# Kernel optimization log

Measured on AMD Instinct MI355X. Metric: run time of the kernel, lower is better.

Reference implementation:

```python
import jax, jax.numpy as jnp
import numpy as np

T, B, D, K = 256, 128, 1024, 21
PAD = 0


def setup_inputs() -> dict:
    key = jax.random.key(0)
    k1, k2, k3, k4, k5, k6, k7 = jax.random.split(key, 7)
    lstm_features = jax.random.normal(k1, (T, B, D), dtype=jnp.float32)
    # gold tags: non-pad (1..K-1) for a random prefix, PAD afterwards; mask[0] all on
    tags = jax.random.randint(k2, (T, B), 1, K)
    lengths = jax.random.randint(k3, (B,), T // 2, T + 1)
    tags = jnp.where(jnp.arange(T)[:, None] < lengths[None, :], tags, PAD)
    W = jax.random.normal(k4, (D, K), dtype=jnp.float32) * 0.02
    b = jnp.zeros((K,), dtype=jnp.float32)
    # torchcrf initializes transitions uniform(-0.1, 0.1)
    start_transitions = jax.random.uniform(k5, (K,), minval=-0.1, maxval=0.1)
    end_transitions = jax.random.uniform(k6, (K,), minval=-0.1, maxval=0.1)
    transitions = jax.random.uniform(k7, (K, K), minval=-0.1, maxval=0.1)
    return {
        'lstm_features': lstm_features,
        'tags': tags,
        'W': W,
        'b': b,
        'start_transitions': start_transitions,
        'end_transitions': end_transitions,
        'transitions': transitions,
    }


def _crf_nll(emissions, tags, mask, start, end, trans):
    # emissions: (T,B,K), tags/mask: (T,B). Returns -sum_b log p(tags|emissions)
    maskf = mask.astype(emissions.dtype)
    # --- numerator: score of gold path (fully vectorized over t) ---
    em_score = jnp.take_along_axis(emissions, tags[:, :, None], axis=2)[:, :, 0]  # (T,B)
    tr_score = trans[tags[:-1], tags[1:]]                                          # (T-1,B)
    num = start[tags[0]] + em_score[0]
    num = num + jnp.sum((tr_score + em_score[1:]) * maskf[1:], axis=0)
    seq_ends = jnp.sum(mask.astype(jnp.int32), axis=0) - 1                         # (B,)
    last_tags = jnp.take_along_axis(tags, seq_ends[None, :], axis=0)[0]
    num = num + end[last_tags]
    # --- denominator: forward algorithm (log partition) via scan ---
    def step(score, xs):  # score: (B,K)
        emit_t, mask_t = xs
        nxt = jax.nn.logsumexp(score[:, :, None] + trans[None, :, :] + emit_t[:, None, :], axis=1)
        return jnp.where(mask_t[:, None], nxt, score), None
    score0 = start[None, :] + emissions[0]
    scoreT, _ = jax.lax.scan(step, score0, (emissions[1:], mask[1:]))
    den = jax.nn.logsumexp(scoreT + end[None, :], axis=1)                          # (B,)
    return -jnp.sum(num - den)


def _viterbi(emissions, mask, start, end, trans):
    # returns best tag sequence (T,B) int32, padded positions set to PAD
    n_tags = emissions.shape[-1]
    ident = jnp.arange(n_tags, dtype=jnp.int32)[None, :]
    def step(score, xs):  # score: (B,K)
        emit_t, mask_t = xs
        cand = score[:, :, None] + trans[None, :, :]          # (B, prev K, next K)
        best_prev = jnp.argmax(cand, axis=1).astype(jnp.int32)  # (B,K)
        nxt = jnp.max(cand, axis=1) + emit_t
        ptr = jnp.where(mask_t[:, None], best_prev, ident)    # identity ptr on padding
        new_score = jnp.where(mask_t[:, None], nxt, score)
        return new_score, ptr
    score0 = start[None, :] + emissions[0]
    scoreT, history = jax.lax.scan(step, score0, (emissions[1:], mask[1:]))  # history: (T-1,B,K)
    last_tag = jnp.argmax(scoreT + end[None, :], axis=1).astype(jnp.int32)   # (B,)
    def back(tag, hist_t):
        prev = jnp.take_along_axis(hist_t, tag[:, None], axis=1)[:, 0]
        return prev, tag
    first_tag, rest = jax.lax.scan(back, last_tag, history, reverse=True)    # rest = tags[1:]
    best = jnp.concatenate([first_tag[None, :], rest], axis=0)               # (T,B)
    return jnp.where(mask, best, PAD)


def reference(lstm_features, tags, W, b, start_transitions, end_transitions, transitions):
    # Linear projection; dropout is identity at inference
    fc_out = jnp.einsum('tbd,dk->tbk', lstm_features, W) + b
    mask = tags != PAD
    crf_out = _viterbi(fc_out, mask, start_transitions, end_transitions, transitions)
    crf_loss = _crf_nll(fc_out, tags, mask, start_transitions, end_transitions, transitions)
    return crf_out, crf_loss
```

## Files before the change

### kernel.cpp

```cpp
#include <hip/hip_runtime.h>
#include <math.h>

#define T_ 256
#define B_ 128
#define D_ 1024
#define K_ 21
#define NB3 43

typedef short v8s __attribute__((ext_vector_type(8)));
typedef float v4f __attribute__((ext_vector_type(4)));

__device__ __forceinline__ short bf16rne(float f) {
  unsigned u = __float_as_uint(f);
  u += 0x7FFFu + ((u >> 16) & 1u);
  return (short)(u >> 16);
}
__device__ __forceinline__ float rdl(float v, int l) {
  return __int_as_float(__builtin_amdgcn_readlane(__float_as_int(v), l));
}
__device__ __forceinline__ int imax3(int a, int b, int c) {
  const int t = a > b ? a : b;
  return t > c ? t : c;
}

typedef const __attribute__((address_space(1))) void* gas1_t;
typedef __attribute__((address_space(3))) void* las3_t;
__device__ __forceinline__ void gload_lds(const float* g, float* l) {
  __builtin_amdgcn_global_load_lds((gas1_t)g, (las3_t)l, 4, 0, 0);
}

__global__ __launch_bounds__(256) void fc_kernel(
    const float* __restrict__ A, const float* __restrict__ W,
    const float* __restrict__ bias, float* __restrict__ fc,
    float* __restrict__ out_loss) {
  __shared__ float red[3][64][22];
  if (blockIdx.x == 0 && threadIdx.x == 0) *out_loss = 0.f;
  const int lane = threadIdx.x & 63;
  const int wv = threadIdx.x >> 6;
  const int m15 = lane & 15, g4 = lane >> 4;
  const int rowbase = blockIdx.x * 64;
  const int kc = wv * 256;
  const int n1 = 16 + m15;

  v8s bf[8][2];
#pragma unroll
  for (int s = 0; s < 8; ++s) {
    const float* Wp = W + (size_t)(kc + 32 * s + 8 * g4) * K_;
#pragma unroll
    for (int j = 0; j < 8; ++j) bf[s][0][j] = bf16rne(Wp[j * K_ + m15]);
    if (n1 < K_) {
#pragma unroll
      for (int j = 0; j < 8; ++j) bf[s][1][j] = bf16rne(Wp[j * K_ + n1]);
    } else {
#pragma unroll
      for (int j = 0; j < 8; ++j) bf[s][1][j] = 0;
    }
  }

  v4f acc[4][2];
#pragma unroll
  for (int m = 0; m < 4; ++m) {
    acc[m][0] = (v4f)(0.f);
    acc[m][1] = (v4f)(0.f);
  }

#pragma unroll
  for (int s = 0; s < 8; ++s) {
    v8s av[4];
#pragma unroll
    for (int m = 0; m < 4; ++m) {
      const float* Ap =
          A + (size_t)(rowbase + 16 * m + m15) * D_ + kc + 32 * s + 8 * g4;
      const float4 x = *(const float4*)Ap;
      const float4 y = *(const float4*)(Ap + 4);
      av[m][0] = bf16rne(x.x); av[m][1] = bf16rne(x.y);
      av[m][2] = bf16rne(x.z); av[m][3] = bf16rne(x.w);
      av[m][4] = bf16rne(y.x); av[m][5] = bf16rne(y.y);
      av[m][6] = bf16rne(y.z); av[m][7] = bf16rne(y.w);
    }
#pragma unroll
    for (int m = 0; m < 4; ++m) {
      acc[m][0] = __builtin_amdgcn_mfma_f32_16x16x32_bf16(av[m], bf[s][0],
                                                          acc[m][0], 0, 0, 0);
      acc[m][1] = __builtin_amdgcn_mfma_f32_16x16x32_bf16(av[m], bf[s][1],
                                                          acc[m][1], 0, 0, 0);
    }
  }

  if (wv > 0) {
#pragma unroll
    for (int m = 0; m < 4; ++m)
#pragma unroll
      for (int ri = 0; ri < 4; ++ri) {
        const int rl = 16 * m + 4 * g4 + ri;
        red[wv - 1][rl][m15] = acc[m][0][ri];
        if (n1 < K_) red[wv - 1][rl][n1] = acc[m][1][ri];
      }
  }
  __syncthreads();
  if (wv == 0) {
    const float b0 = bias[m15];
    const float b1 = (n1 < K_) ? bias[n1] : 0.f;
#pragma unroll
    for (int m = 0; m < 4; ++m)
#pragma unroll
      for (int ri = 0; ri < 4; ++ri) {
        const int rl = 16 * m + 4 * g4 + ri;
        float* o = fc + (size_t)(rowbase + rl) * K_;
        o[m15] = acc[m][0][ri] + red[0][rl][m15] + red[1][rl][m15] +
                 red[2][rl][m15] + b0;
        if (n1 < K_)
          o[n1] = acc[m][1][ri] + red[0][rl][n1] + red[1][rl][n1] +
                  red[2][rl][n1] + b1;
      }
  }
}

__global__ __launch_bounds__(64) void scan_kernel(
    const float* __restrict__ fc, const int* __restrict__ tags,
    const float* __restrict__ startT, const float* __restrict__ endT,
    const float* __restrict__ trans, float* __restrict__ out_tags,
    float* __restrict__ out_loss) {
  __shared__ v4f statev[18];
  __shared__ float fcs[2][32][64];
  __shared__ unsigned short bp[256 * 66];
  __shared__ unsigned char h2[127 * 66];
  __shared__ unsigned char h4[63 * 66];
  __shared__ unsigned char cur[3 * 256];

  const int lane = threadIdx.x;
  const int blk = blockIdx.x;

  if (blk < 2 * NB3) {
    const bool fwd = blk < NB3;
    const int bblk = fwd ? blk : blk - NB3;
    int g = lane / 21;
    if (g > 2) g = 2;
    int jloc = lane - g * 21;
    if (jloc > 20) jloc = 20;
    const int gj = g * 21 + jloc;
    const int b0 = bblk * 3;

    int len0 = 0, len1 = 0, len2 = 0;
#pragma unroll
    for (int q = 0; q < 4; ++q) {
      const int t = q * 64 + lane;
      int bb0 = b0, bb1 = b0 + 1, bb2 = b0 + 2;
      if (bb1 >= B_) bb1 = B_ - 1;
      if (bb2 >= B_) bb2 = B_ - 1;
      len0 += __popcll(__ballot(tags[t * B_ + bb0] != 0));
      len1 += __popcll(__ballot(tags[t * B_ + bb1] != 0));
      len2 += __popcll(__ballot(tags[t * B_ + bb2] != 0));
    }
    const int mylen = (g == 0) ? len0 : (g == 1) ? len1 : len2;

    float* sb = (float*)statev + g * 24;
    const v4f* sv = (const v4f*)sb;

#define STAGE(c)                                                             \
    {                                                                        \
      const float* src_ = fc + ((size_t)((c) * 32) * B_ + b0) * K_ + lane;   \
      float* dst_ = &fcs[(c) & 1][0][0];                                     \
      _Pragma("unroll")                                                      \
      for (int q_ = 0; q_ < 32; ++q_)                                        \
        gload_lds(src_ + (size_t)q_ * (B_ * K_), dst_ + q_ * 64);            \
    }
#define WAIT_VM0()                                                           \
    {                                                                        \
      asm volatile("s_waitcnt vmcnt(0)" ::: "memory");                       \
      __builtin_amdgcn_sched_barrier(0);                                     \
    }

    STAGE(0)
    WAIT_VM0()
    const float em0 = fcs[0][0][gj];
    STAGE(1)

    if (fwd) {
      float ec[21];
#pragma unroll
      for (int i = 0; i < K_; ++i) ec[i] = __expf(trans[i * K_ + jloc]);
      float p = __expf(startT[jloc] + em0);
      sb[jloc] = p;
      float L = 0.f;

      for (int c = 0; c < 8; ++c) {
        const float* fb = &fcs[c & 1][0][0];
        const int t1 = c * 32 + 32;
        for (int t = c ? c * 32 : 1; t < t1; ++t) {
          const float emt = fb[(t & 31) * 64 + gj];
          const v4f A0 = sv[0], A1 = sv[1], A2 = sv[2], A3 = sv[3],
                    A4 = sv[4];
          const float A5 = sb[20];

          float d0 = A0[0] * ec[0], d1 = A0[1] * ec[1], d2 = A0[2] * ec[2];
          d0 = fmaf(A0[3], ec[3], d0); d1 = fmaf(A1[0], ec[4], d1);
          d2 = fmaf(A1[1], ec[5], d2);
          d0 = fmaf(A1[2], ec[6], d0); d1 = fmaf(A1[3], ec[7], d1);
          d2 = fmaf(A2[0], ec[8], d2);
          d0 = fmaf(A2[1], ec[9], d0); d1 = fmaf(A2[2], ec[10], d1);
          d2 = fmaf(A2[3], ec[11], d2);
          d0 = fmaf(A3[0], ec[12], d0); d1 = fmaf(A3[1], ec[13], d1);
          d2 = fmaf(A3[2], ec[14], d2);
          d0 = fmaf(A3[3], ec[15], d0); d1 = fmaf(A4[0], ec[16], d1);
          d2 = fmaf(A4[1], ec[17], d2);
          d0 = fmaf(A4[2], ec[18], d0); d1 = fmaf(A4[3], ec[19], d1);
          d2 = fmaf(A5, ec[20], d2);

          const float pn = ((d0 + d1) + d2) * __expf(emt);
          p = (t < mylen) ? pn : p;
          if ((t & 7) == 0) {
            const float f = A0[0];
            p *= __builtin_amdgcn_rcpf(f);
            L += __logf(f);
          }
          sb[jloc] = p;
        }
        if (c < 7) {
          WAIT_VM0()
          if (c + 2 < 8) STAGE(c + 2)
        }
      }

      const float w = p * __expf(endT[jloc]);
      float res = 0.f;
#pragma unroll
      for (int gg = 0; gg < 3; ++gg) {
        if (b0 + gg < B_) {
          float tot = 0.f;
#pragma unroll
          for (int i = 0; i < K_; ++i) tot += rdl(w, gg * K_ + i);
          res += rdl(L, gg * K_) + __logf(tot);
        }
      }
      if (lane == 0) atomicAdd(out_loss, res);
    } else {
      float tr[21];
#pragma unroll
      for (int i = 0; i < K_; ++i) tr[i] = trans[i * K_ + jloc] + 2048.0f;
      float sc = startT[jloc] + em0;
      sb[jloc] = sc;

      for (int c = 0; c < 8; ++c) {
        const float* fb = &fcs[c & 1][0][0];
        const int t1 = c * 32 + 32;
        for (int t = c ? c * 32 : 1; t < t1; ++t) {
          const float emt = fb[(t & 31) * 64 + gj];
          const v4f A0 = sv[0], A1 = sv[1], A2 = sv[2], A3 = sv[3],
                    A4 = sv[4];
          const float A5 = sb[20];

#define KEY(i, V) ((__float_as_int((V) + tr[i]) & 0xFFFFFFE0) | (20 - (i)))
          const int q0 = imax3(KEY(0, A0[0]), KEY(1, A0[1]), KEY(2, A0[2]));
          const int q1 = imax3(KEY(3, A0[3]), KEY(4, A1[0]), KEY(5, A1[1]));
          const int q2 = imax3(KEY(6, A1[2]), KEY(7, A1[3]), KEY(8, A2[0]));
          const int q3 = imax3(KEY(9, A2[1]), KEY(10, A2[2]), KEY(11, A2[3]));
          const int q4 = imax3(KEY(12, A3[0]), KEY(13, A3[1]), KEY(14, A3[2]));
          const int q5 = imax3(KEY(15, A3[3]), KEY(16, A4[0]), KEY(17, A4[1]));
          const int q6 = imax3(KEY(18, A4[2]), KEY(19, A4[3]), KEY(20, A5));
          const int km = imax3(imax3(q0, q1, q2), imax3(q3, q4, q5), q6);
#undef KEY
          const float nxt = __int_as_float(km & 0xFFFFFFE0) - 2048.0f + emt;
          const bool m = t < mylen;
          sc = m ? nxt : sc;
          sb[jloc] = sc;
          const int pw = m ? (20 - (km & 31)) : jloc;
          bp[t * 66 + g * 22 + jloc] = (unsigned short)pw;
        }
        if (c < 7) {
          WAIT_VM0()
          if (c + 2 < 8) STAGE(c + 2)
        }
      }
      __syncthreads();

      const float finb = sc + endT[jloc] + 2048.0f;
      const int myk = (__float_as_int(finb) & 0xFFFFFFE0) | (20 - jloc);
      int last0 = 0, last1 = 0, last2 = 0;
#pragma unroll
      for (int gg = 0; gg < 3; ++gg) {
        int km = 0;
#pragma unroll
        for (int i = 0; i < K_; ++i) {
          const int ki = __builtin_amdgcn_readlane(myk, gg * K_ + i);
          km = km > ki ? km : ki;
        }
        const int lt = 20 - (km & 31);
        if (gg == 0) last0 = lt;
        else if (gg == 1) last1 = lt;
        else last2 = lt;
      }

      for (int i = lane; i < 127 * 63; i += 64) {
        const int v = i / 63;
        const int rem = i - v * 63;
        const int gg = rem / 21, j = rem - (rem / 21) * 21;
        h2[v * 66 + gg * 22 + j] = (unsigned char)
            bp[(2 * v + 1) * 66 + gg * 22 + bp[(2 * v + 2) * 66 + gg * 22 + j]];
      }
      __syncthreads();
      for (int i = lane; i < 63 * 63; i += 64) {
        const int w = i / 63;
        const int rem = i - w * 63;
        const int gg = rem / 21, j = rem - (rem / 21) * 21;
        h4[w * 66 + gg * 22 + j] =
            h2[(2 * w) * 66 + gg * 22 + h2[(2 * w + 1) * 66 + gg * 22 + j]];
      }
      __syncthreads();

      if (lane < 3 && b0 + lane < B_) {
        int c = (lane == 0) ? last0 : (lane == 1) ? last1 : last2;
        cur[lane * 256 + 255] = (unsigned char)c;
        c = bp[255 * 66 + lane * 22 + c];
        cur[lane * 256 + 254] = (unsigned char)c;
        c = h2[126 * 66 + lane * 22 + c];
        cur[lane * 256 + 252] = (unsigned char)c;
        for (int w = 62; w >= 0; --w) {
          c = h4[w * 66 + lane * 22 + c];
          cur[lane * 256 + 4 * w] = (unsigned char)c;
        }
      }
      __syncthreads();
      for (int i = lane; i < 63 * 3; i += 64) {
        const int gg = i / 63, ii = i - (i / 63) * 63;
        const int t = 2 + 4 * ii;
        cur[gg * 256 + t] =
            h2[(t >> 1) * 66 + gg * 22 + cur[gg * 256 + t + 2]];
      }
      __syncthreads();
      for (int i = lane; i < 127 * 3; i += 64) {
        const int gg = i / 127, ii = i - (i / 127) * 127;
        const int t = 1 + 2 * ii;
        cur[gg * 256 + t] = (unsigned char)
            bp[(t + 1) * 66 + gg * 22 + cur[gg * 256 + t + 1]];
      }
      __syncthreads();
      for (int i = lane; i < 3 * 256; i += 64) {
        const int gg = i >> 8, t = i & 255;
        const int bb = b0 + gg;
        const int lg = (gg == 0) ? len0 : (gg == 1) ? len1 : len2;
        if (bb < B_)
          out_tags[t * B_ + bb] = (t < lg) ? (float)cur[gg * 256 + t] : 0.f;
      }
    }
#undef STAGE
#undef WAIT_VM0
  } else {
    const int b = blk - 2 * NB3;
    float contrib = 0.f;
#pragma unroll
    for (int q = 0; q < 4; ++q) {
      const int t = lane * 4 + q;
      const int tg = tags[t * B_ + b];
      const size_t ro = ((size_t)t * B_ + b) * K_;
      if (t == 0) {
        contrib += startT[tg] + fc[ro + tg];
      } else if (tg != 0) {
        const int pg = tags[(t - 1) * B_ + b];
        contrib += trans[pg * K_ + tg] + fc[ro + tg];
      }
      const bool isLast =
          (tg != 0) && (t == T_ - 1 || tags[(t + 1) * B_ + b] == 0);
      if (isLast) contrib += endT[tg];
    }
#pragma unroll
    for (int off = 32; off > 0; off >>= 1)
      contrib += __shfl_down(contrib, off, 64);
    if (lane == 0) atomicAdd(out_loss, -contrib);
  }
}

extern "C" void kernel_launch(void* const* d_in, const int* in_sizes, int n_in,
                              void* d_out, int out_size, void* d_ws,
                              size_t ws_size, hipStream_t stream) {
  const float* A = (const float*)d_in[0];
  const int* tags = (const int*)d_in[1];
  const float* W = (const float*)d_in[2];
  const float* bias = (const float*)d_in[3];
  const float* startT = (const float*)d_in[4];
  const float* endT = (const float*)d_in[5];
  const float* trans = (const float*)d_in[6];

  float* out_tags = (float*)d_out;
  float* out_loss = (float*)d_out + (size_t)T_ * B_;
  float* fc = (float*)d_ws;

  fc_kernel<<<512, 256, 0, stream>>>(A, W, bias, fc, out_loss);
  scan_kernel<<<2 * NB3 + B_, 64, 0, stream>>>(fc, tags, startT, endT, trans,
                                               out_tags, out_loss);
}
```

Measured before the change: 280.8 us.

## Fuse projection GEMM with CRF scans in one wave-specialized producer-consumer kernel

Replaces the separate projection kernel and scan kernel with a single kernel of 43 blocks. In each block, two waves compute the bf16 MFMA projection chunk by chunk into double-buffered LDS. Two other waves run the forward and Viterbi recurrences at the same time, synchronized through LDS flags. This removes the global round trip of the emission matrix and the second launch, and overlaps the memory-bound projection with the latency-bound serial scan. The cost is that the 128 MB input is now streamed by only 86 waves across 43 CUs. The loss reset also relies on a global magic-value flag that stays set from earlier calls, which may race on repeated launches.

New measurement: 486.0 us. 1.73x slower.

```diff
diff --git a/kernel.cpp b/kernel.cpp
--- a/kernel.cpp
+++ b/kernel.cpp
@@ -5,7 +5,8 @@
 #define B_ 128
 #define D_ 1024
 #define K_ 21
-#define NB3 43
+#define NBLK 43
+#define MAGIC64 0xA3C59B17E4D2F861ull
 
 typedef short v8s __attribute__((ext_vector_type(8)));
 typedef float v4f __attribute__((ext_vector_type(4)));
@@ -22,351 +23,358 @@
   const int t = a > b ? a : b;
   return t > c ? t : c;
 }
-
-typedef const __attribute__((address_space(1))) void* gas1_t;
-typedef __attribute__((address_space(3))) void* las3_t;
-__device__ __forceinline__ void gload_lds(const float* g, float* l) {
-  __builtin_amdgcn_global_load_lds((gas1_t)g, (las3_t)l, 4, 0, 0);
-}
-
-__global__ __launch_bounds__(256) void fc_kernel(
+__device__ __forceinline__ int cvt2(float lo, float hi) {
+  int r;
+  asm("v_cvt_pk_bf16_f32 %0, %1, %2" : "=v"(r) : "v"(lo), "v"(hi));
+  return r;
+}
+__device__ __forceinline__ void lds_wait(int* f) {
+  while (__hip_atomic_load(f, __ATOMIC_RELAXED, __HIP_MEMORY_SCOPE_WORKGROUP) == 0)
+    __builtin_amdgcn_s_sleep(1);
+}
+__device__ __forceinline__ void lds_set(int* f) {
+  __hip_atomic_store(f, 1, __ATOMIC_RELAXED, __HIP_MEMORY_SCOPE_WORKGROUP);
+}
+
+__global__ __launch_bounds__(256) void crf_kernel(
     const float* __restrict__ A, const float* __restrict__ W,
-    const float* __restrict__ bias, float* __restrict__ fc,
-    float* __restrict__ out_loss) {
-  __shared__ float red[3][64][22];
-  if (blockIdx.x == 0 && threadIdx.x == 0) *out_loss = 0.f;
-  const int lane = threadIdx.x & 63;
-  const int wv = threadIdx.x >> 6;
-  const int m15 = lane & 15, g4 = lane >> 4;
-  const int rowbase = blockIdx.x * 64;
-  const int kc = wv * 256;
-  const int n1 = 16 + m15;
-
-  v8s bf[8][2];
-#pragma unroll
-  for (int s = 0; s < 8; ++s) {
-    const float* Wp = W + (size_t)(kc + 32 * s + 8 * g4) * K_;
-#pragma unroll
-    for (int j = 0; j < 8; ++j) bf[s][0][j] = bf16rne(Wp[j * K_ + m15]);
-    if (n1 < K_) {
-#pragma unroll
-      for (int j = 0; j < 8; ++j) bf[s][1][j] = bf16rne(Wp[j * K_ + n1]);
-    } else {
-#pragma unroll
-      for (int j = 0; j < 8; ++j) bf[s][1][j] = 0;
-    }
-  }
-
-  v4f acc[4][2];
-#pragma unroll
-  for (int m = 0; m < 4; ++m) {
-    acc[m][0] = (v4f)(0.f);
-    acc[m][1] = (v4f)(0.f);
-  }
-
-#pragma unroll
-  for (int s = 0; s < 8; ++s) {
-    v8s av[4];
-#pragma unroll
-    for (int m = 0; m < 4; ++m) {
-      const float* Ap =
-          A + (size_t)(rowbase + 16 * m + m15) * D_ + kc + 32 * s + 8 * g4;
-      const float4 x = *(const float4*)Ap;
-      const float4 y = *(const float4*)(Ap + 4);
-      av[m][0] = bf16rne(x.x); av[m][1] = bf16rne(x.y);
-      av[m][2] = bf16rne(x.z); av[m][3] = bf16rne(x.w);
-      av[m][4] = bf16rne(y.x); av[m][5] = bf16rne(y.y);
-      av[m][6] = bf16rne(y.z); av[m][7] = bf16rne(y.w);
-    }
-#pragma unroll
-    for (int m = 0; m < 4; ++m) {
-      acc[m][0] = __builtin_amdgcn_mfma_f32_16x16x32_bf16(av[m], bf[s][0],
-                                                          acc[m][0], 0, 0, 0);
-      acc[m][1] = __builtin_amdgcn_mfma_f32_16x16x32_bf16(av[m], bf[s][1],
-                                                          acc[m][1], 0, 0, 0);
-    }
-  }
-
-  if (wv > 0) {
-#pragma unroll
-    for (int m = 0; m < 4; ++m)
-#pragma unroll
-      for (int ri = 0; ri < 4; ++ri) {
-        const int rl = 16 * m + 4 * g4 + ri;
-        red[wv - 1][rl][m15] = acc[m][0][ri];
-        if (n1 < K_) red[wv - 1][rl][n1] = acc[m][1][ri];
-      }
-  }
-  __syncthreads();
-  if (wv == 0) {
-    const float b0 = bias[m15];
-    const float b1 = (n1 < K_) ? bias[n1] : 0.f;
-#pragma unroll
-    for (int m = 0; m < 4; ++m)
-#pragma unroll
-      for (int ri = 0; ri < 4; ++ri) {
-        const int rl = 16 * m + 4 * g4 + ri;
-        float* o = fc + (size_t)(rowbase + rl) * K_;
-        o[m15] = acc[m][0][ri] + red[0][rl][m15] + red[1][rl][m15] +
-                 red[2][rl][m15] + b0;
-        if (n1 < K_)
-          o[n1] = acc[m][1][ri] + red[0][rl][n1] + red[1][rl][n1] +
-                  red[2][rl][n1] + b1;
-      }
-  }
-}
-
-__global__ __launch_bounds__(64) void scan_kernel(
-    const float* __restrict__ fc, const int* __restrict__ tags,
+    const float* __restrict__ bias, const int* __restrict__ tags,
     const float* __restrict__ startT, const float* __restrict__ endT,
     const float* __restrict__ trans, float* __restrict__ out_tags,
-    float* __restrict__ out_loss) {
-  __shared__ v4f statev[18];
+    float* __restrict__ out_loss, unsigned long long* __restrict__ readyg) {
   __shared__ float fcs[2][32][64];
+  __shared__ unsigned short Wt[21 * 1032];
   __shared__ unsigned short bp[256 * 66];
   __shared__ unsigned char h2[127 * 66];
   __shared__ unsigned char h4[63 * 66];
   __shared__ unsigned char cur[3 * 256];
-
-  const int lane = threadIdx.x;
+  __shared__ float stateF[3 * 24], stateV[3 * 24];
+  __shared__ int flg[5][8];
+
+  const int tix = threadIdx.x;
+  const int lane = tix & 63;
+  const int wv = tix >> 6;
   const int blk = blockIdx.x;
-
-  if (blk < 2 * NB3) {
-    const bool fwd = blk < NB3;
-    const int bblk = fwd ? blk : blk - NB3;
-    int g = lane / 21;
-    if (g > 2) g = 2;
-    int jloc = lane - g * 21;
-    if (jloc > 20) jloc = 20;
-    const int gj = g * 21 + jloc;
-    const int b0 = bblk * 3;
-
-    int len0 = 0, len1 = 0, len2 = 0;
-#pragma unroll
-    for (int q = 0; q < 4; ++q) {
-      const int t = q * 64 + lane;
-      int bb0 = b0, bb1 = b0 + 1, bb2 = b0 + 2;
-      if (bb1 >= B_) bb1 = B_ - 1;
-      if (bb2 >= B_) bb2 = B_ - 1;
-      len0 += __popcll(__ballot(tags[t * B_ + bb0] != 0));
-      len1 += __popcll(__ballot(tags[t * B_ + bb1] != 0));
-      len2 += __popcll(__ballot(tags[t * B_ + bb2] != 0));
-    }
-    const int mylen = (g == 0) ? len0 : (g == 1) ? len1 : len2;
-
-    float* sb = (float*)statev + g * 24;
+  const int b0 = blk * 3;
+
+  if (tix < 40) ((int*)flg)[tix] = 0;
+  if (blk == 0 && tix == 0) {
+    atomicExch(out_loss, 0.f);
+    __builtin_amdgcn_fence(__ATOMIC_RELEASE, "agent");
+    __hip_atomic_store(readyg, MAGIC64, __ATOMIC_RELAXED,
+                       __HIP_MEMORY_SCOPE_AGENT);
+  }
+  for (int i = tix; i < K_ * D_; i += 256) {
+    const int k = i / K_, c = i - (i / K_) * K_;
+    Wt[c * 1032 + k] = (unsigned short)bf16rne(W[i]);
+  }
+
+  int len0 = 0, len1 = 0, len2 = 0;
+#pragma unroll
+  for (int q = 0; q < 4; ++q) {
+    const int t = q * 64 + lane;
+    int bb0 = b0, bb1 = b0 + 1, bb2 = b0 + 2;
+    if (bb1 >= B_) bb1 = B_ - 1;
+    if (bb2 >= B_) bb2 = B_ - 1;
+    len0 += __popcll(__ballot(tags[t * B_ + bb0] != 0));
+    len1 += __popcll(__ballot(tags[t * B_ + bb1] != 0));
+    len2 += __popcll(__ballot(tags[t * B_ + bb2] != 0));
+  }
+  __syncthreads();
+
+  int g = lane / 21;
+  if (g > 2) g = 2;
+  int jloc = lane - g * 21;
+  if (jloc > 20) jloc = 20;
+  const int gj = g * 21 + jloc;
+  const int mylen = (g == 0) ? len0 : (g == 1) ? len1 : len2;
+  int last0 = 0, last1 = 0, last2 = 0;
+
+  if (wv == 0) {
+    float* sb = stateF + g * 24;
     const v4f* sv = (const v4f*)sb;
-
-#define STAGE(c)                                                             \
-    {                                                                        \
-      const float* src_ = fc + ((size_t)((c) * 32) * B_ + b0) * K_ + lane;   \
-      float* dst_ = &fcs[(c) & 1][0][0];                                     \
-      _Pragma("unroll")                                                      \
-      for (int q_ = 0; q_ < 32; ++q_)                                        \
-        gload_lds(src_ + (size_t)q_ * (B_ * K_), dst_ + q_ * 64);            \
-    }
-#define WAIT_VM0()                                                           \
-    {                                                                        \
-      asm volatile("s_waitcnt vmcnt(0)" ::: "memory");                       \
-      __builtin_amdgcn_sched_barrier(0);                                     \
-    }
-
-    STAGE(0)
-    WAIT_VM0()
-    const float em0 = fcs[0][0][gj];
-    STAGE(1)
-
-    if (fwd) {
-      float ec[21];
-#pragma unroll
-      for (int i = 0; i < K_; ++i) ec[i] = __expf(trans[i * K_ + jloc]);
-      float p = __expf(startT[jloc] + em0);
-      sb[jloc] = p;
-      float L = 0.f;
-
-      for (int c = 0; c < 8; ++c) {
-        const float* fb = &fcs[c & 1][0][0];
-        const int t1 = c * 32 + 32;
-        for (int t = c ? c * 32 : 1; t < t1; ++t) {
-          const float emt = fb[(t & 31) * 64 + gj];
-          const v4f A0 = sv[0], A1 = sv[1], A2 = sv[2], A3 = sv[3],
-                    A4 = sv[4];
-          const float A5 = sb[20];
-
-          float d0 = A0[0] * ec[0], d1 = A0[1] * ec[1], d2 = A0[2] * ec[2];
-          d0 = fmaf(A0[3], ec[3], d0); d1 = fmaf(A1[0], ec[4], d1);
-          d2 = fmaf(A1[1], ec[5], d2);
-          d0 = fmaf(A1[2], ec[6], d0); d1 = fmaf(A1[3], ec[7], d1);
-          d2 = fmaf(A2[0], ec[8], d2);
-          d0 = fmaf(A2[1], ec[9], d0); d1 = fmaf(A2[2], ec[10], d1);
-          d2 = fmaf(A2[3], ec[11], d2);
-          d0 = fmaf(A3[0], ec[12], d0); d1 = fmaf(A3[1], ec[13], d1);
-          d2 = fmaf(A3[2], ec[14], d2);
-          d0 = fmaf(A3[3], ec[15], d0); d1 = fmaf(A4[0], ec[16], d1);
-          d2 = fmaf(A4[1], ec[17], d2);
-          d0 = fmaf(A4[2], ec[18], d0); d1 = fmaf(A4[3], ec[19], d1);
-          d2 = fmaf(A5, ec[20], d2);
-
-          const float pn = ((d0 + d1) + d2) * __expf(emt);
-          p = (t < mylen) ? pn : p;
-          if ((t & 7) == 0) {
-            const float f = A0[0];
-            p *= __builtin_amdgcn_rcpf(f);
-            L += __logf(f);
+    float ec[21];
+#pragma unroll
+    for (int i = 0; i < K_; ++i) ec[i] = __expf(trans[i * K_ + jloc]);
+    float p = 0.f, L = 0.f;
+
+    for (int c = 0; c < 8; ++c) {
+      lds_wait(&flg[0][c]);
+      lds_wait(&flg[1][c]);
+      const float* fb = &fcs[c & 1][0][0];
+      int t0 = c * 32;
+      if (c == 0) {
+        p = __expf(startT[jloc] + fb[gj]);
+        sb[jloc] = p;
+        t0 = 1;
+      }
+      const int t1 = c * 32 + 32;
+      for (int t = t0; t < t1; ++t) {
+        const float emt = fb[(t & 31) * 64 + gj];
+        const v4f A0 = sv[0], A1 = sv[1], A2 = sv[2], A3 = sv[3], A4 = sv[4];
+        const float A5 = sb[20];
+
+        float d0 = A0[0] * ec[0], d1 = A0[1] * ec[1], d2 = A0[2] * ec[2];
+        d0 = fmaf(A0[3], ec[3], d0); d1 = fmaf(A1[0], ec[4], d1);
+        d2 = fmaf(A1[1], ec[5], d2);
+        d0 = fmaf(A1[2], ec[6], d0); d1 = fmaf(A1[3], ec[7], d1);
+        d2 = fmaf(A2[0], ec[8], d2);
+        d0 = fmaf(A2[1], ec[9], d0); d1 = fmaf(A2[2], ec[10], d1);
+        d2 = fmaf(A2[3], ec[11], d2);
+        d0 = fmaf(A3[0], ec[12], d0); d1 = fmaf(A3[1], ec[13], d1);
+        d2 = fmaf(A3[2], ec[14], d2);
+        d0 = fmaf(A3[3], ec[15], d0); d1 = fmaf(A4[0], ec[16], d1);
+        d2 = fmaf(A4[1], ec[17], d2);
+        d0 = fmaf(A4[2], ec[18], d0); d1 = fmaf(A4[3], ec[19], d1);
+        d2 = fmaf(A5, ec[20], d2);
+
+        const float pn = ((d0 + d1) + d2) * __expf(emt);
+        p = (t < mylen) ? pn : p;
+        if ((t & 7) == 0) {
+          const float f = A0[0];
+          p *= __builtin_amdgcn_rcpf(f);
+          L += __logf(f);
+        }
+        sb[jloc] = p;
+      }
+      lds_set(&flg[2][c]);
+    }
+
+    const float w = p * __expf(endT[jloc]);
+    float res = 0.f;
+#pragma unroll
+    for (int gg = 0; gg < 3; ++gg) {
+      if (b0 + gg < B_) {
+        float tot = 0.f;
+#pragma unroll
+        for (int i = 0; i < K_; ++i) tot += rdl(w, gg * K_ + i);
+        res += rdl(L, gg * K_) + __logf(tot);
+      }
+    }
+    if (lane == 0) {
+      while (__hip_atomic_load(readyg, __ATOMIC_RELAXED,
+                               __HIP_MEMORY_SCOPE_AGENT) != MAGIC64)
+        __builtin_amdgcn_s_sleep(4);
+      __builtin_amdgcn_fence(__ATOMIC_ACQUIRE, "agent");
+      atomicAdd(out_loss, res);
+    }
+  } else if (wv == 1) {
+    float* sb = stateV + g * 24;
+    const v4f* sv = (const v4f*)sb;
+    float tr[21];
+#pragma unroll
+    for (int i = 0; i < K_; ++i) tr[i] = trans[i * K_ + jloc] + 2048.0f;
+    float sc = 0.f;
+
+    for (int c = 0; c < 8; ++c) {
+      lds_wait(&flg[0][c]);
+      lds_wait(&flg[1][c]);
+      const float* fb = &fcs[c & 1][0][0];
+      int t0 = c * 32;
+      if (c == 0) {
+        sc = startT[jloc] + fb[gj];
+        sb[jloc] = sc;
+        t0 = 1;
+      }
+      const int t1 = c * 32 + 32;
+      for (int t = t0; t < t1; ++t) {
+        const float emt = fb[(t & 31) * 64 + gj];
+        const v4f A0 = sv[0], A1 = sv[1], A2 = sv[2], A3 = sv[3], A4 = sv[4];
+        const float A5 = sb[20];
+
+#define KEY(i, V) ((__float_as_int((V) + tr[i]) & 0xFFFFFFE0) | (20 - (i)))
+        const int q0 = imax3(KEY(0, A0[0]), KEY(1, A0[1]), KEY(2, A0[2]));
+        const int q1 = imax3(KEY(3, A0[3]), KEY(4, A1[0]), KEY(5, A1[1]));
+        const int q2 = imax3(KEY(6, A1[2]), KEY(7, A1[3]), KEY(8, A2[0]));
+        const int q3 = imax3(KEY(9, A2[1]), KEY(10, A2[2]), KEY(11, A2[3]));
+        const int q4 = imax3(KEY(12, A3[0]), KEY(13, A3[1]), KEY(14, A3[2]));
+        const int q5 = imax3(KEY(15, A3[3]), KEY(16, A4[0]), KEY(17, A4[1]));
+        const int q6 = imax3(KEY(18, A4[2]), KEY(19, A4[3]), KEY(20, A5));
+        const int km = imax3(imax3(q0, q1, q2), imax3(q3, q4, q5), q6);
+#undef KEY
+        const float nxt = __int_as_float(km & 0xFFFFFFE0) - 2048.0f + emt;
+        const bool m = t < mylen;
+        sc = m ? nxt : sc;
+        sb[jloc] = sc;
+        const int pw = m ? (20 - (km & 31)) : jloc;
+        bp[t * 66 + g * 22 + jloc] = (unsigned short)pw;
+      }
+      lds_set(&flg[3][c]);
+    }
+
+    const float finb = sc + endT[jloc] + 2048.0f;
+    const int myk = (__float_as_int(finb) & 0xFFFFFFE0) | (20 - jloc);
+#pragma unroll
+    for (int gg = 0; gg < 3; ++gg) {
+      int km = 0;
+#pragma unroll
+      for (int i = 0; i < K_; ++i) {
+        const int ki = __builtin_amdgcn_readlane(myk, gg * K_ + i);
+        km = km > ki ? km : ki;
+      }
+      const int lt = 20 - (km & 31);
+      if (gg == 0) last0 = lt;
+      else if (gg == 1) last1 = lt;
+      else last2 = lt;
+    }
+  } else {
+    const int wid = wv - 2;
+    const int m15 = lane & 15, g4 = lane >> 4;
+    const float bias0 = bias[m15];
+    const float bias1 = (m15 < 5) ? bias[16 + m15] : 0.f;
+    int ggm[3], tbase[3];
+    size_t abase[3];
+#pragma unroll
+    for (int m = 0; m < 3; ++m) {
+      const int mt = 3 * wid + m;
+      ggm[m] = mt >> 1;
+      tbase[m] = (mt & 1) * 16;
+      int bb = b0 + ggm[m];
+      if (bb >= B_) bb = B_ - 1;
+      abase[m] = ((size_t)(tbase[m] + m15) * B_ + bb) * D_ + 8 * g4;
+    }
+    float numacc = 0.f;
+
+    for (int c = 0; c < 8; ++c) {
+      if (c >= 2) {
+        lds_wait(&flg[2][c - 2]);
+        lds_wait(&flg[3][c - 2]);
+        lds_wait(&flg[4][c - 2]);
+      }
+      v4f acc[3][2];
+#pragma unroll
+      for (int m = 0; m < 3; ++m) {
+        acc[m][0] = (v4f)(0.f);
+        acc[m][1] = (v4f)(0.f);
+      }
+      const size_t coff = (size_t)c * 32 * B_ * D_;
+#pragma unroll 2
+      for (int ks = 0; ks < 32; ++ks) {
+        const int wo = 32 * ks + 8 * g4;
+        const v8s bf0 = *(const v8s*)&Wt[m15 * 1032 + wo];
+        v8s bf1;
+        if (m15 < 5) {
+          bf1 = *(const v8s*)&Wt[(16 + m15) * 1032 + wo];
+        } else {
+#pragma unroll
+          for (int j = 0; j < 8; ++j) bf1[j] = 0;
+        }
+#pragma unroll
+        for (int m = 0; m < 3; ++m) {
+          const float* Ap = A + abase[m] + coff + 32 * ks;
+          const float4 x = *(const float4*)Ap;
+          const float4 y = *(const float4*)(Ap + 4);
+          union { int4 i4; v8s s8; } u;
+          u.i4.x = cvt2(x.x, x.y);
+          u.i4.y = cvt2(x.z, x.w);
+          u.i4.z = cvt2(y.x, y.y);
+          u.i4.w = cvt2(y.z, y.w);
+          acc[m][0] = __builtin_amdgcn_mfma_f32_16x16x32_bf16(u.s8, bf0,
+                                                              acc[m][0], 0, 0, 0);
+          acc[m][1] = __builtin_amdgcn_mfma_f32_16x16x32_bf16(u.s8, bf1,
+                                                              acc[m][1], 0, 0, 0);
+        }
+      }
+      float* fb = &fcs[c & 1][0][0];
+#pragma unroll
+      for (int m = 0; m < 3; ++m) {
+        const int cb = ggm[m] * 21;
+#pragma unroll
+        for (int ri = 0; ri < 4; ++ri) {
+          const int tl = tbase[m] + 4 * g4 + ri;
+          fb[tl * 64 + cb + m15] = acc[m][0][ri] + bias0;
+          if (m15 < 5) fb[tl * 64 + cb + 16 + m15] = acc[m][1][ri] + bias1;
+        }
+      }
+      lds_set(&flg[wid][c]);
+
+      if (wid == 0) {
+        lds_wait(&flg[1][c]);
+        if (lane < 32) {
+          const int t = c * 32 + lane;
+#pragma unroll
+          for (int gg = 0; gg < 3; ++gg) {
+            const int bb = b0 + gg;
+            if (bb < B_) {
+              const int tg = tags[t * B_ + bb];
+              if (t == 0) {
+                numacc += startT[tg] + fb[gg * 21 + tg];
+              } else if (tg != 0) {
+                const int pg = tags[(t - 1) * B_ + bb];
+                numacc += trans[pg * K_ + tg] + fb[(t & 31) * 64 + gg * 21 + tg];
+              }
+              if (tg != 0 && (t == T_ - 1 || tags[(t + 1) * B_ + bb] == 0))
+                numacc += endT[tg];
+            }
           }
-          sb[jloc] = p;
-        }
-        if (c < 7) {
-          WAIT_VM0()
-          if (c + 2 < 8) STAGE(c + 2)
-        }
-      }
-
-      const float w = p * __expf(endT[jloc]);
-      float res = 0.f;
-#pragma unroll
-      for (int gg = 0; gg < 3; ++gg) {
-        if (b0 + gg < B_) {
-          float tot = 0.f;
-#pragma unroll
-          for (int i = 0; i < K_; ++i) tot += rdl(w, gg * K_ + i);
-          res += rdl(L, gg * K_) + __logf(tot);
-        }
-      }
-      if (lane == 0) atomicAdd(out_loss, res);
-    } else {
-      float tr[21];
-#pragma unroll
-      for (int i = 0; i < K_; ++i) tr[i] = trans[i * K_ + jloc] + 2048.0f;
-      float sc = startT[jloc] + em0;
-      sb[jloc] = sc;
-
-      for (int c = 0; c < 8; ++c) {
-        const float* fb = &fcs[c & 1][0][0];
-        const int t1 = c * 32 + 32;
-        for (int t = c ? c * 32 : 1; t < t1; ++t) {
-          const float emt = fb[(t & 31) * 64 + gj];
-          const v4f A0 = sv[0], A1 = sv[1], A2 = sv[2], A3 = sv[3],
-                    A4 = sv[4];
-          const float A5 = sb[20];
-
-#define KEY(i, V) ((__float_as_int((V) + tr[i]) & 0xFFFFFFE0) | (20 - (i)))
-          const int q0 = imax3(KEY(0, A0[0]), KEY(1, A0[1]), KEY(2, A0[2]));
-          const int q1 = imax3(KEY(3, A0[3]), KEY(4, A1[0]), KEY(5, A1[1]));
-          const int q2 = imax3(KEY(6, A1[2]), KEY(7, A1[3]), KEY(8, A2[0]));
-          const int q3 = imax3(KEY(9, A2[1]), KEY(10, A2[2]), KEY(11, A2[3]));
-          const int q4 = imax3(KEY(12, A3[0]), KEY(13, A3[1]), KEY(14, A3[2]));
-          const int q5 = imax3(KEY(15, A3[3]), KEY(16, A4[0]), KEY(17, A4[1]));
-          const int q6 = imax3(KEY(18, A4[2]), KEY(19, A4[3]), KEY(20, A5));
-          const int km = imax3(imax3(q0, q1, q2), imax3(q3, q4, q5), q6);
-#undef KEY
-          const float nxt = __int_as_float(km & 0xFFFFFFE0) - 2048.0f + emt;
-          const bool m = t < mylen;
-          sc = m ? nxt : sc;
-          sb[jloc] = sc;
-          const int pw = m ? (20 - (km & 31)) : jloc;
-          bp[t * 66 + g * 22 + jloc] = (unsigned short)pw;
-        }
-        if (c < 7) {
-          WAIT_VM0()
-          if (c + 2 < 8) STAGE(c + 2)
-        }
-      }
-      __syncthreads();
-
-      const float finb = sc + endT[jloc] + 2048.0f;
-      const int myk = (__float_as_int(finb) & 0xFFFFFFE0) | (20 - jloc);
-      int last0 = 0, last1 = 0, last2 = 0;
-#pragma unroll
-      for (int gg = 0; gg < 3; ++gg) {
-        int km = 0;
-#pragma unroll
-        for (int i = 0; i < K_; ++i) {
-          const int ki = __builtin_amdgcn_readlane(myk, gg * K_ + i);
-          km = km > ki ? km : ki;
-        }
-        const int lt = 20 - (km & 31);
-        if (gg == 0) last0 = lt;
-        else if (gg == 1) last1 = lt;
-        else last2 = lt;
-      }
-
-      for (int i = lane; i < 127 * 63; i += 64) {
-        const int v = i / 63;
-        const int rem = i - v * 63;
-        const int gg = rem / 21, j = rem - (rem / 21) * 21;
-        h2[v * 66 + gg * 22 + j] = (unsigned char)
-            bp[(2 * v + 1) * 66 + gg * 22 + bp[(2 * v + 2) * 66 + gg * 22 + j]];
-      }
-      __syncthreads();
-      for (int i = lane; i < 63 * 63; i += 64) {
-        const int w = i / 63;
-        const int rem = i - w * 63;
-        const int gg = rem / 21, j = rem - (rem / 21) * 21;
-        h4[w * 66 + gg * 22 + j] =
-            h2[(2 * w) * 66 + gg * 22 + h2[(2 * w + 1) * 66 + gg * 22 + j]];
-      }
-      __syncthreads();
-
-      if (lane < 3 && b0 + lane < B_) {
-        int c = (lane == 0) ? last0 : (lane == 1) ? last1 : last2;
-        cur[lane * 256 + 255] = (unsigned char)c;
-        c = bp[255 * 66 + lane * 22 + c];
-        cur[lane * 256 + 254] = (unsigned char)c;
-        c = h2[126 * 66 + lane * 22 + c];
-        cur[lane * 256 + 252] = (unsigned char)c;
-        for (int w = 62; w >= 0; --w) {
-          c = h4[w * 66 + lane * 22 + c];
-          cur[lane * 256 + 4 * w] = (unsigned char)c;
-        }
-      }
-      __syncthreads();
-      for (int i = lane; i < 63 * 3; i += 64) {
-        const int gg = i / 63, ii = i - (i / 63) * 63;
-        const int t = 2 + 4 * ii;
-        cur[gg * 256 + t] =
-            h2[(t >> 1) * 66 + gg * 22 + cur[gg * 256 + t + 2]];
-      }
-      __syncthreads();
-      for (int i = lane; i < 127 * 3; i += 64) {
-        const int gg = i / 127, ii = i - (i / 127) * 127;
-        const int t = 1 + 2 * ii;
-        cur[gg * 256 + t] = (unsigned char)
-            bp[(t + 1) * 66 + gg * 22 + cur[gg * 256 + t + 1]];
-      }
-      __syncthreads();
-      for (int i = lane; i < 3 * 256; i += 64) {
-        const int gg = i >> 8, t = i & 255;
-        const int bb = b0 + gg;
-        const int lg = (gg == 0) ? len0 : (gg == 1) ? len1 : len2;
-        if (bb < B_)
-          out_tags[t * B_ + bb] = (t < lg) ? (float)cur[gg * 256 + t] : 0.f;
-      }
-    }
-#undef STAGE
-#undef WAIT_VM0
-  } else {
-    const int b = blk - 2 * NB3;
-    float contrib = 0.f;
-#pragma unroll
-    for (int q = 0; q < 4; ++q) {
-      const int t = lane * 4 + q;
-      const int tg = tags[t * B_ + b];
-      const size_t ro = ((size_t)t * B_ + b) * K_;
-      if (t == 0) {
-        contrib += startT[tg] + fc[ro + tg];
-      } else if (tg != 0) {
-        const int pg = tags[(t - 1) * B_ + b];
-        contrib += trans[pg * K_ + tg] + fc[ro + tg];
-      }
-      const bool isLast =
-          (tg != 0) && (t == T_ - 1 || tags[(t + 1) * B_ + b] == 0);
-      if (isLast) contrib += endT[tg];
-    }
-#pragma unroll
-    for (int off = 32; off > 0; off >>= 1)
-      contrib += __shfl_down(contrib, off, 64);
-    if (lane == 0) atomicAdd(out_loss, -contrib);
+        }
+        lds_set(&flg[4][c]);
+      }
+    }
+    if (wid == 0) {
+#pragma unroll
+      for (int off = 32; off > 0; off >>= 1)
+        numacc += __shfl_down(numacc, off, 64);
+      if (lane == 0) {
+        while (__hip_atomic_load(readyg, __ATOMIC_RELAXED,
+                                 __HIP_MEMORY_SCOPE_AGENT) != MAGIC64)
+          __builtin_amdgcn_s_sleep(4);
+        __builtin_amdgcn_fence(__ATOMIC_ACQUIRE, "agent");
+        atomicAdd(out_loss, -numacc);
+      }
+    }
+  }
+
+  __syncthreads();
+  for (int i = tix; i < 127 * 63; i += 256) {
+    const int v = i / 63;
+    const int rem = i - v * 63;
+    const int gg = rem / 21, j = rem - (rem / 21) * 21;
+    h2[v * 66 + gg * 22 + j] = (unsigned char)
+        bp[(2 * v + 1) * 66 + gg * 22 + bp[(2 * v + 2) * 66 + gg * 22 + j]];
+  }
+  __syncthreads();
+  for (int i = tix; i < 63 * 63; i += 256) {
+    const int w2 = i / 63;
+    const int rem = i - w2 * 63;
+    const int gg = rem / 21, j = rem - (rem / 21) * 21;
+    h4[w2 * 66 + gg * 22 + j] =
+        h2[(2 * w2) * 66 + gg * 22 + h2[(2 * w2 + 1) * 66 + gg * 22 + j]];
+  }
+  __syncthreads();
+
+  if (wv == 1 && lane < 3 && b0 + lane < B_) {
+    int c = (lane == 0) ? last0 : (lane == 1) ? last1 : last2;
+    cur[lane * 256 + 255] = (unsigned char)c;
+    c = bp[255 * 66 + lane * 22 + c];
+    cur[lane * 256 + 254] = (unsigned char)c;
+    c = h2[126 * 66 + lane * 22 + c];
+    cur[lane * 256 + 252] = (unsigned char)c;
+    for (int w2 = 62; w2 >= 0; --w2) {
+      c = h4[w2 * 66 + lane * 22 + c];
+      cur[lane * 256 + 4 * w2] = (unsigned char)c;
+    }
+  }
+  __syncthreads();
+  for (int i = tix; i < 63 * 3; i += 256) {
+    const int gg = i / 63, ii = i - (i / 63) * 63;
+    const int t = 2 + 4 * ii;
+    cur[gg * 256 + t] = h2[(t >> 1) * 66 + gg * 22 + cur[gg * 256 + t + 2]];
+  }
+  __syncthreads();
+  for (int i = tix; i < 127 * 3; i += 256) {
+    const int gg = i / 127, ii = i - (i / 127) * 127;
+    const int t = 1 + 2 * ii;
+    cur[gg * 256 + t] =
+        (unsigned char)bp[(t + 1) * 66 + gg * 22 + cur[gg * 256 + t + 1]];
+  }
+  __syncthreads();
+  for (int i = tix; i < 3 * 256; i += 256) {
+    const int gg = i >> 8, t = i & 255;
+    const int bb = b0 + gg;
+    const int lg = (gg == 0) ? len0 : (gg == 1) ? len1 : len2;
+    if (bb < B_)
+      out_tags[t * B_ + bb] = (t < lg) ? (float)cur[gg * 256 + t] : 0.f;
   }
 }
 
@@ -383,9 +391,8 @@
 
   float* out_tags = (float*)d_out;
   float* out_loss = (float*)d_out + (size_t)T_ * B_;
-  float* fc = (float*)d_ws;
-
-  fc_kernel<<<512, 256, 0, stream>>>(A, W, bias, fc, out_loss);
-  scan_kernel<<<2 * NB3 + B_, 64, 0, stream>>>(fc, tags, startT, endT, trans,
-                                               out_tags, out_loss);
-}
+  unsigned long long* readyg = (unsigned long long*)d_ws;
+
+  crf_kernel<<<NBLK, 256, 0, stream>>>(A, W, bias, tags, startT, endT, trans,
+                                       out_tags, out_loss, readyg);
+}
```
